# Optimization experiments

Measured on AMD Instinct MI355X. Metric: run time of the kernel, lower is better.

The kernel has to match this reference:

```python
import jax, jax.numpy as jnp
import numpy as np

K = 10          # neighbors, hard-coded in MLP1.forward
NEG_SLOPE = 0.2 # LeakyReLU slope
EPS = 1e-5      # BatchNorm2d default eps


def setup_inputs() -> dict:
    key = jax.random.key(0)
    k1, k2, k3, k4 = jax.random.split(key, 4)
    B, C, N = 8, 6, 4096
    x = jax.random.normal(k1, (B, C, N), dtype=jnp.float32)
    W = jax.random.normal(k2, (64, 6), dtype=jnp.float32) * 0.2      # conv1x1 weight (O, I)
    gamma = jax.random.uniform(k3, (64,), jnp.float32, 0.5, 1.5)     # BN weight
    beta = jax.random.normal(k4, (64,), dtype=jnp.float32) * 0.1     # BN bias
    return {"x": x, "W": W, "gamma": gamma, "beta": beta}


def _knn_idx(x3, k):
    # pairwise_distance[b,i,j] = -||x_i - x_j||^2 (as in the torch knn)
    inner = jnp.einsum('bdn,bdm->bnm', x3, x3)          # x_i . x_j
    xx = jnp.sum(x3 * x3, axis=1)                       # (B, N)
    pd = 2.0 * inner - xx[:, :, None] - xx[:, None, :]  # (B, N, N)
    _, idx = jax.lax.top_k(pd, k)                       # k nearest (incl. self)
    return idx                                          # (B, N, k) int32


def reference(x, W, gamma, beta):
    # x: (B, 6, N)
    idx = _knn_idx(x[:, :3], K)                          # (B, N, k)
    # gather neighbor features: feat[b,c,n,j] = x[b,c,idx[b,n,j]]
    feat = jax.vmap(lambda xb, ib: xb[:, ib])(x, idx)    # (B, 6, N, k)
    # center xyz over the k neighbors and scale by 10
    xyz = feat[:, :3]
    xyz = (xyz - jnp.mean(xyz, axis=-1, keepdims=True)) * 10.0
    feat = jnp.concatenate([xyz, feat[:, 3:]], axis=1)   # (B, 6, N, k)
    # 1x1 conv (6 -> 64), no bias
    y = jnp.einsum('oc,bcnk->bonk', W, feat)             # (B, 64, N, k)
    # BatchNorm2d in train mode: batch stats over (B, N, k), biased variance
    mu = jnp.mean(y, axis=(0, 2, 3), keepdims=True)
    var = jnp.mean((y - mu) ** 2, axis=(0, 2, 3), keepdims=True)
    y = (y - mu) * jax.lax.rsqrt(var + EPS)
    y = y * gamma[None, :, None, None] + beta[None, :, None, None]
    # LeakyReLU(0.2)
    y = jnp.where(y >= 0, y, NEG_SLOPE * y)
    # max over neighbors k
    y = jnp.max(y, axis=-1)                              # (B, 64, N)
    # global max + mean pooling over N, concat along last axis
    x1 = jnp.max(y, axis=-1)                             # (B, 64)
    x2 = jnp.mean(y, axis=-1)                            # (B, 64)
    return jnp.concatenate([x1, x2], axis=-1)            # (B, 128)
```

## Files before the change

kernel.cpp:

```cpp
#include <hip/hip_runtime.h>
#include <float.h>

#define K_NN 10
#define BATCH 8
#define CIN 6
#define NPTS 4096
#define COUT 64
#define NSEG 8
#define SEGLEN (NPTS / NSEG)
#define CHUNK 16
#define NCHUNK (SEGLEN / CHUNK)
#define CAP 32
#define NEG_SLOPE 0.2f
#define BN_EPS 1e-5f

static constexpr size_t OFF_IDX = 0;
static constexpr size_t OFF_PTS = OFF_IDX + (size_t)BATCH * K_NN * NPTS * sizeof(int);
static constexpr size_t OFF_Q   = OFF_PTS + (size_t)BATCH * NPTS * sizeof(float4);
static constexpr size_t SZ_Q    = (size_t)NSEG * BATCH * NPTS * K_NN * sizeof(int);
static constexpr size_t OFF_ST  = OFF_Q + SZ_Q;
static constexpr size_t OFF_SS  = OFF_ST + 32 * sizeof(double);

__device__ __forceinline__ float wave_sum(float v) {
#pragma unroll
    for (int m = 32; m >= 1; m >>= 1) v += __shfl_xor(v, m, 64);
    return v;
}
__device__ __forceinline__ float wave_max(float v) {
#pragma unroll
    for (int m = 32; m >= 1; m >>= 1) v = fmaxf(v, __shfl_xor(v, m, 64));
    return v;
}

__device__ __forceinline__ float distp(float4 qp, float4 c) {
    return fmaf(2.0f, fmaf(qp.z, c.z, fmaf(qp.y, c.y, qp.x * c.x)), -c.w);
}

__global__ __launch_bounds__(256) void prep_pts(const float* __restrict__ x,
                                                float4* __restrict__ pts,
                                                double* __restrict__ stats) {
    if (blockIdx.x == 0 && threadIdx.x < 27) stats[threadIdx.x] = 0.0;
    int t = blockIdx.x * 256 + threadIdx.x;
    int b = t >> 12;
    int n = t & (NPTS - 1);
    const float* xb = x + (size_t)b * CIN * NPTS;
    float x0 = xb[n];
    float x1 = xb[NPTS + n];
    float x2 = xb[2 * NPTS + n];
    pts[t] = make_float4(x0, x1, x2, x0 * x0 + x1 * x1 + x2 * x2);
}

__global__ __launch_bounds__(256) void knn_part(const float4* __restrict__ pts,
                                                int* __restrict__ part) {
    __shared__ unsigned short ssm[CAP * 256];
    int b = blockIdx.y;
    int s = blockIdx.z;
    int n = blockIdx.x * 256 + threadIdx.x;
    const float4* p = pts + (size_t)b * NPTS;
    float4 qp = p[n];

    int m0 = s * SEGLEN;

    float vals[K_NN];
#pragma unroll
    for (int j = 0; j < K_NN; j++) vals[j] = -FLT_MAX;

    for (int ch = 0; ch < NCHUNK; ch++) {
        float cmax = -FLT_MAX;
#pragma unroll
        for (int u = 0; u < CHUNK; u++) {
            float4 c = p[m0 + ch * CHUNK + u];
            cmax = fmaxf(cmax, distp(qp, c));
        }
        float t = cmax;
#pragma unroll
        for (int j = 0; j < K_NN; j++) {
            float hi = fmaxf(vals[j], t);
            t = fminf(vals[j], t);
            vals[j] = hi;
        }
    }
    float thr = vals[K_NN - 1];

    int cnt = 0;
#pragma unroll 8
    for (int mm = 0; mm < SEGLEN; mm++) {
        float4 c = p[m0 + mm];
        float d = distp(qp, c);
        int slot = min(cnt, CAP - 1);
        ssm[slot * 256 + threadIdx.x] = (unsigned short)(m0 + mm);
        cnt += (d >= thr) ? 1 : 0;
    }

    float fv[K_NN];
    int fi[K_NN];
#pragma unroll
    for (int j = 0; j < K_NN; j++) { fv[j] = -FLT_MAX; fi[j] = 0; }

    if (cnt <= CAP) {
        for (int j = 0; j < cnt; j++) {
            int m = ssm[j * 256 + threadIdx.x];
            float4 c = p[m];
            float d = distp(qp, c);
            if (d > fv[K_NN - 1]) {
                fv[K_NN - 1] = d;
                fi[K_NN - 1] = m;
#pragma unroll
                for (int t2 = K_NN - 1; t2 > 0; t2--) {
                    if (fv[t2] > fv[t2 - 1]) {
                        float tv = fv[t2]; fv[t2] = fv[t2 - 1]; fv[t2 - 1] = tv;
                        int ti = fi[t2]; fi[t2] = fi[t2 - 1]; fi[t2 - 1] = ti;
                    }
                }
            }
        }
    } else {
        for (int mm = 0; mm < SEGLEN; mm++) {
            int m = m0 + mm;
            float4 c = p[m];
            float d = distp(qp, c);
            if (d > fv[K_NN - 1]) {
                fv[K_NN - 1] = d;
                fi[K_NN - 1] = m;
#pragma unroll
                for (int t2 = K_NN - 1; t2 > 0; t2--) {
                    if (fv[t2] > fv[t2 - 1]) {
                        float tv = fv[t2]; fv[t2] = fv[t2 - 1]; fv[t2 - 1] = tv;
                        int ti = fi[t2]; fi[t2] = fi[t2 - 1]; fi[t2 - 1] = ti;
                    }
                }
            }
        }
    }

    int* o = part + (((size_t)s * BATCH + b) * K_NN) * NPTS + n;
#pragma unroll
    for (int j = 0; j < K_NN; j++) o[(size_t)j * NPTS] = fi[j];
}

__global__ __launch_bounds__(256) void merge_kernel(const float4* __restrict__ pts,
                                                    const int* __restrict__ part,
                                                    int* __restrict__ idxo) {
    int b = blockIdx.y;
    int n = blockIdx.x * 256 + threadIdx.x;
    const float4* p = pts + (size_t)b * NPTS;
    float4 qp = p[n];

    float vals[K_NN];
    int inds[K_NN];
#pragma unroll
    for (int j = 0; j < K_NN; j++) { vals[j] = -FLT_MAX; inds[j] = 0; }

#pragma unroll
    for (int s = 0; s < NSEG; s++) {
        const int* pp = part + (((size_t)s * BATCH + b) * K_NN) * NPTS + n;
#pragma unroll
        for (int j = 0; j < K_NN; j++) {
            int m = pp[(size_t)j * NPTS];
            float4 c = p[m];
            float d = distp(qp, c);
            if (d > vals[K_NN - 1]) {
                vals[K_NN - 1] = d;
                inds[K_NN - 1] = m;
#pragma unroll
                for (int t = K_NN - 1; t > 0; t--) {
                    if (vals[t] > vals[t - 1]) {
                        float tv = vals[t]; vals[t] = vals[t - 1]; vals[t - 1] = tv;
                        int ti = inds[t]; inds[t] = inds[t - 1]; inds[t - 1] = ti;
                    }
                }
            }
        }
    }

    int* o = idxo + (size_t)b * K_NN * NPTS + n;
#pragma unroll
    for (int j = 0; j < K_NN; j++) o[(size_t)j * NPTS] = inds[j];
}

__global__ __launch_bounds__(256) void feat_kernel(const float4* __restrict__ pts,
                                                   const float* __restrict__ x,
                                                   const float* __restrict__ W,
                                                   const int* __restrict__ idx,
                                                   float* __restrict__ q,
                                                   double* __restrict__ stats) {
    __shared__ float sW[COUT * CIN];
    __shared__ float sred[4][27];
    for (int i = threadIdx.x; i < COUT * CIN; i += 256) sW[i] = W[i];
    __syncthreads();

    int b = blockIdx.y;
    int n = blockIdx.x * 256 + threadIdx.x;
    const float* xb = x + (size_t)b * CIN * NPTS;
    const float4* p = pts + (size_t)b * NPTS;

    int nb[K_NN];
#pragma unroll
    for (int k = 0; k < K_NN; k++) nb[k] = idx[((size_t)b * K_NN + k) * NPTS + n];

    float f[CIN][K_NN];
#pragma unroll
    for (int k = 0; k < K_NN; k++) {
        float4 c = p[nb[k]];
        f[0][k] = c.x; f[1][k] = c.y; f[2][k] = c.z;
    }
#pragma unroll
    for (int c = 3; c < CIN; c++)
#pragma unroll
        for (int k = 0; k < K_NN; k++)
            f[c][k] = xb[c * NPTS + nb[k]];

#pragma unroll
    for (int c = 0; c < 3; c++) {
        float s = 0.f;
#pragma unroll
        for (int k = 0; k < K_NN; k++) s += f[c][k];
        float m = s / 10.0f;
#pragma unroll
        for (int k = 0; k < K_NN; k++) f[c][k] = (f[c][k] - m) * 10.0f;
    }

    float* qb = q + (size_t)b * COUT * NPTS + n;
#pragma unroll
    for (int o = 0; o < COUT; o++) {
        float w0 = sW[o * 6 + 0], w1 = sW[o * 6 + 1], w2 = sW[o * 6 + 2];
        float w3 = sW[o * 6 + 3], w4 = sW[o * 6 + 4], w5 = sW[o * 6 + 5];
        float mx = -FLT_MAX;
#pragma unroll
        for (int k = 0; k < K_NN; k++) {
            float y = w0 * f[0][k] + w1 * f[1][k] + w2 * f[2][k] +
                      w3 * f[3][k] + w4 * f[4][k] + w5 * f[5][k];
            mx = fmaxf(mx, y);
        }
        qb[(size_t)o * NPTS] = mx;
    }

    float s1[CIN];
#pragma unroll
    for (int c = 0; c < CIN; c++) {
        float s = 0.f;
#pragma unroll
        for (int k = 0; k < K_NN; k++) s += f[c][k];
        s1[c] = s;
    }
    float s2[21];
#pragma unroll
    for (int i = 0; i < 21; i++) s2[i] = 0.f;
#pragma unroll
    for (int k = 0; k < K_NN; k++) {
        int pp = 0;
#pragma unroll
        for (int c = 0; c < CIN; c++)
#pragma unroll
            for (int c2 = c; c2 < CIN; c2++) {
                s2[pp] += f[c][k] * f[c2][k];
                pp++;
            }
    }
#pragma unroll
    for (int c = 0; c < CIN; c++) s1[c] = wave_sum(s1[c]);
#pragma unroll
    for (int i = 0; i < 21; i++) s2[i] = wave_sum(s2[i]);

    int wv = threadIdx.x >> 6;
    int ln = threadIdx.x & 63;
    if (ln == 0) {
#pragma unroll
        for (int c = 0; c < CIN; c++) sred[wv][c] = s1[c];
#pragma unroll
        for (int i = 0; i < 21; i++) sred[wv][6 + i] = s2[i];
    }
    __syncthreads();
    if (threadIdx.x < 27) {
        float t = sred[0][threadIdx.x] + sred[1][threadIdx.x] +
                  sred[2][threadIdx.x] + sred[3][threadIdx.x];
        atomicAdd(&stats[threadIdx.x], (double)t);
    }
}

__global__ void stats_kernel(const double* __restrict__ stats,
                             const float* __restrict__ W,
                             const float* __restrict__ gamma,
                             const float* __restrict__ beta,
                             float* __restrict__ ss) {
    int o = threadIdx.x;
    const double minv = 1.0 / (double)((size_t)BATCH * NPTS * K_NN);
    double w[CIN];
#pragma unroll
    for (int c = 0; c < CIN; c++) w[c] = (double)W[o * CIN + c];
    double mu = 0.0;
#pragma unroll
    for (int c = 0; c < CIN; c++) mu += w[c] * stats[c];
    mu *= minv;
    double ey2 = 0.0;
    int p = 6;
#pragma unroll
    for (int c = 0; c < CIN; c++)
#pragma unroll
        for (int c2 = c; c2 < CIN; c2++) {
            double v = w[c] * w[c2] * stats[p];
            ey2 += (c2 == c) ? v : 2.0 * v;
            p++;
        }
    ey2 *= minv;
    double var = ey2 - mu * mu;
    float scale = gamma[o] * rsqrtf((float)var + BN_EPS);
    float shift = beta[o] - (float)mu * scale;
    ss[o] = scale;
    ss[COUT + o] = shift;
}

__global__ __launch_bounds__(256) void reduce_kernel(const float* __restrict__ q,
                                                     const float* __restrict__ ss,
                                                     float* __restrict__ out) {
    int o = blockIdx.x;
    int b = blockIdx.y;
    const float* qp = q + ((size_t)b * COUT + o) * NPTS;
    float scale = ss[o], shift = ss[COUT + o];
    float mx = -FLT_MAX, sm = 0.f;
    for (int i = threadIdx.x; i < NPTS; i += 256) {
        float z = scale * qp[i] + shift;
        z = (z >= 0.f) ? z : NEG_SLOPE * z;
        mx = fmaxf(mx, z);
        sm += z;
    }
    mx = wave_max(mx);
    sm = wave_sum(sm);
    __shared__ float smx[4], ssm2[4];
    int wv = threadIdx.x >> 6;
    int ln = threadIdx.x & 63;
    if (ln == 0) { smx[wv] = mx; ssm2[wv] = sm; }
    __syncthreads();
    if (threadIdx.x == 0) {
        float m = fmaxf(fmaxf(smx[0], smx[1]), fmaxf(smx[2], smx[3]));
        float s = ssm2[0] + ssm2[1] + ssm2[2] + ssm2[3];
        out[b * 2 * COUT + o] = m;
        out[b * 2 * COUT + COUT + o] = s * (1.0f / (float)NPTS);
    }
}

extern "C" void kernel_launch(void* const* d_in, const int* in_sizes, int n_in,
                              void* d_out, int out_size, void* d_ws, size_t ws_size,
                              hipStream_t stream) {
    const float* x     = (const float*)d_in[0];
    const float* W     = (const float*)d_in[1];
    const float* gamma = (const float*)d_in[2];
    const float* beta  = (const float*)d_in[3];
    float* out = (float*)d_out;

    char* ws = (char*)d_ws;
    int*    idx   = (int*)(ws + OFF_IDX);
    float4* pts   = (float4*)(ws + OFF_PTS);
    int*    part  = (int*)(ws + OFF_Q);
    float*  q     = (float*)(ws + OFF_Q);
    double* stats = (double*)(ws + OFF_ST);
    float*  ss    = (float*)(ws + OFF_SS);

    prep_pts<<<BATCH * NPTS / 256, 256, 0, stream>>>(x, pts, stats);
    knn_part<<<dim3(NPTS / 256, BATCH, NSEG), 256, 0, stream>>>(pts, part);
    merge_kernel<<<dim3(NPTS / 256, BATCH), 256, 0, stream>>>(pts, part, idx);
    feat_kernel<<<dim3(NPTS / 256, BATCH), 256, 0, stream>>>(pts, x, W, idx, q, stats);
    stats_kernel<<<1, COUT, 0, stream>>>(stats, W, gamma, beta, ss);
    reduce_kernel<<<dim3(COUT, BATCH), 256, 0, stream>>>(q, ss, out);
}
```

Baseline: 197.5 us.

## Fuse kNN merge into feature kernel with wave-split merging and packed features

```diff
diff --git a/kernel.cpp b/kernel.cpp
--- a/kernel.cpp
+++ b/kernel.cpp
@@ -11,15 +11,16 @@
 #define CHUNK 16
 #define NCHUNK (SEGLEN / CHUNK)
 #define CAP 32
+#define PPB 64
 #define NEG_SLOPE 0.2f
 #define BN_EPS 1e-5f
 
-static constexpr size_t OFF_IDX = 0;
-static constexpr size_t OFF_PTS = OFF_IDX + (size_t)BATCH * K_NN * NPTS * sizeof(int);
-static constexpr size_t OFF_Q   = OFF_PTS + (size_t)BATCH * NPTS * sizeof(float4);
-static constexpr size_t SZ_Q    = (size_t)NSEG * BATCH * NPTS * K_NN * sizeof(int);
-static constexpr size_t OFF_ST  = OFF_Q + SZ_Q;
-static constexpr size_t OFF_SS  = OFF_ST + 32 * sizeof(double);
+static constexpr size_t OFF_PTS2 = 0;
+static constexpr size_t OFF_PTS  = OFF_PTS2 + (size_t)BATCH * NPTS * sizeof(float4);
+static constexpr size_t OFF_Q    = OFF_PTS + (size_t)BATCH * NPTS * sizeof(float4);
+static constexpr size_t SZ_Q     = (size_t)BATCH * NSEG * K_NN * NPTS * sizeof(int);
+static constexpr size_t OFF_ST   = OFF_Q + SZ_Q;
+static constexpr size_t OFF_SS   = OFF_ST + 32 * sizeof(double);
 
 __device__ __forceinline__ float wave_sum(float v) {
 #pragma unroll
@@ -36,8 +37,25 @@
     return fmaf(2.0f, fmaf(qp.z, c.z, fmaf(qp.y, c.y, qp.x * c.x)), -c.w);
 }
 
+__device__ __forceinline__ void lex_insert(float (&vals)[K_NN], int (&inds)[K_NN],
+                                           float d, int m) {
+    if (d > vals[K_NN - 1] || (d == vals[K_NN - 1] && m < inds[K_NN - 1])) {
+        vals[K_NN - 1] = d;
+        inds[K_NN - 1] = m;
+#pragma unroll
+        for (int t = K_NN - 1; t > 0; t--) {
+            if (vals[t] > vals[t - 1] ||
+                (vals[t] == vals[t - 1] && inds[t] < inds[t - 1])) {
+                float tv = vals[t]; vals[t] = vals[t - 1]; vals[t - 1] = tv;
+                int ti = inds[t]; inds[t] = inds[t - 1]; inds[t - 1] = ti;
+            }
+        }
+    }
+}
+
 __global__ __launch_bounds__(256) void prep_pts(const float* __restrict__ x,
                                                 float4* __restrict__ pts,
+                                                float4* __restrict__ pts2,
                                                 double* __restrict__ stats) {
     if (blockIdx.x == 0 && threadIdx.x < 27) stats[threadIdx.x] = 0.0;
     int t = blockIdx.x * 256 + threadIdx.x;
@@ -48,11 +66,12 @@
     float x1 = xb[NPTS + n];
     float x2 = xb[2 * NPTS + n];
     pts[t] = make_float4(x0, x1, x2, x0 * x0 + x1 * x1 + x2 * x2);
+    pts2[t] = make_float4(xb[3 * NPTS + n], xb[4 * NPTS + n], xb[5 * NPTS + n], 0.f);
 }
 
 __global__ __launch_bounds__(256) void knn_part(const float4* __restrict__ pts,
                                                 int* __restrict__ part) {
-    __shared__ unsigned short ssm[CAP * 256];
+    __shared__ unsigned int ssm[CAP * 256];
     int b = blockIdx.y;
     int s = blockIdx.z;
     int n = blockIdx.x * 256 + threadIdx.x;
@@ -88,128 +107,90 @@
         float4 c = p[m0 + mm];
         float d = distp(qp, c);
         int slot = min(cnt, CAP - 1);
-        ssm[slot * 256 + threadIdx.x] = (unsigned short)(m0 + mm);
+        ssm[slot * 256 + threadIdx.x] = (unsigned int)(m0 + mm);
         cnt += (d >= thr) ? 1 : 0;
     }
 
     float fv[K_NN];
     int fi[K_NN];
 #pragma unroll
-    for (int j = 0; j < K_NN; j++) { fv[j] = -FLT_MAX; fi[j] = 0; }
+    for (int j = 0; j < K_NN; j++) { fv[j] = -FLT_MAX; fi[j] = 0x7FFFFFFF; }
 
     if (cnt <= CAP) {
         for (int j = 0; j < cnt; j++) {
-            int m = ssm[j * 256 + threadIdx.x];
+            int m = (int)ssm[j * 256 + threadIdx.x];
             float4 c = p[m];
-            float d = distp(qp, c);
-            if (d > fv[K_NN - 1]) {
-                fv[K_NN - 1] = d;
-                fi[K_NN - 1] = m;
-#pragma unroll
-                for (int t2 = K_NN - 1; t2 > 0; t2--) {
-                    if (fv[t2] > fv[t2 - 1]) {
-                        float tv = fv[t2]; fv[t2] = fv[t2 - 1]; fv[t2 - 1] = tv;
-                        int ti = fi[t2]; fi[t2] = fi[t2 - 1]; fi[t2 - 1] = ti;
-                    }
-                }
-            }
+            lex_insert(fv, fi, distp(qp, c), m);
         }
     } else {
         for (int mm = 0; mm < SEGLEN; mm++) {
             int m = m0 + mm;
             float4 c = p[m];
-            float d = distp(qp, c);
-            if (d > fv[K_NN - 1]) {
-                fv[K_NN - 1] = d;
-                fi[K_NN - 1] = m;
-#pragma unroll
-                for (int t2 = K_NN - 1; t2 > 0; t2--) {
-                    if (fv[t2] > fv[t2 - 1]) {
-                        float tv = fv[t2]; fv[t2] = fv[t2 - 1]; fv[t2 - 1] = tv;
-                        int ti = fi[t2]; fi[t2] = fi[t2 - 1]; fi[t2 - 1] = ti;
-                    }
-                }
-            }
-        }
-    }
-
-    int* o = part + (((size_t)s * BATCH + b) * K_NN) * NPTS + n;
+            lex_insert(fv, fi, distp(qp, c), m);
+        }
+    }
+
+    int* o = part + (((size_t)b * NSEG + s) * K_NN) * NPTS + n;
 #pragma unroll
     for (int j = 0; j < K_NN; j++) o[(size_t)j * NPTS] = fi[j];
 }
 
-__global__ __launch_bounds__(256) void merge_kernel(const float4* __restrict__ pts,
-                                                    const int* __restrict__ part,
-                                                    int* __restrict__ idxo) {
+__global__ __launch_bounds__(256) void merge_feat(const float4* __restrict__ pts,
+                                                  const float4* __restrict__ pts2,
+                                                  const float* __restrict__ W,
+                                                  const int* __restrict__ part,
+                                                  float* __restrict__ q,
+                                                  double* __restrict__ stats) {
+    __shared__ float sW[COUT * CIN];
+    __shared__ float ld[4][K_NN][PPB];
+    __shared__ int   li[4][K_NN][PPB];
+    __shared__ float sred[27];
+    for (int i = threadIdx.x; i < COUT * CIN; i += 256) sW[i] = W[i];
+
     int b = blockIdx.y;
-    int n = blockIdx.x * 256 + threadIdx.x;
+    int pt = threadIdx.x & (PPB - 1);
+    int h = threadIdx.x >> 6;
+    int n = blockIdx.x * PPB + pt;
     const float4* p = pts + (size_t)b * NPTS;
+    const float4* p2 = pts2 + (size_t)b * NPTS;
     float4 qp = p[n];
 
     float vals[K_NN];
     int inds[K_NN];
 #pragma unroll
-    for (int j = 0; j < K_NN; j++) { vals[j] = -FLT_MAX; inds[j] = 0; }
-
-#pragma unroll
-    for (int s = 0; s < NSEG; s++) {
-        const int* pp = part + (((size_t)s * BATCH + b) * K_NN) * NPTS + n;
+    for (int j = 0; j < K_NN; j++) { vals[j] = -FLT_MAX; inds[j] = 0x7FFFFFFF; }
+
+#pragma unroll
+    for (int ss = 0; ss < 2; ss++) {
+        int s = h * 2 + ss;
+        const int* pp = part + (((size_t)b * NSEG + s) * K_NN) * NPTS + n;
 #pragma unroll
         for (int j = 0; j < K_NN; j++) {
             int m = pp[(size_t)j * NPTS];
             float4 c = p[m];
-            float d = distp(qp, c);
-            if (d > vals[K_NN - 1]) {
-                vals[K_NN - 1] = d;
-                inds[K_NN - 1] = m;
-#pragma unroll
-                for (int t = K_NN - 1; t > 0; t--) {
-                    if (vals[t] > vals[t - 1]) {
-                        float tv = vals[t]; vals[t] = vals[t - 1]; vals[t - 1] = tv;
-                        int ti = inds[t]; inds[t] = inds[t - 1]; inds[t - 1] = ti;
-                    }
-                }
-            }
-        }
-    }
-
-    int* o = idxo + (size_t)b * K_NN * NPTS + n;
-#pragma unroll
-    for (int j = 0; j < K_NN; j++) o[(size_t)j * NPTS] = inds[j];
-}
-
-__global__ __launch_bounds__(256) void feat_kernel(const float4* __restrict__ pts,
-                                                   const float* __restrict__ x,
-                                                   const float* __restrict__ W,
-                                                   const int* __restrict__ idx,
-                                                   float* __restrict__ q,
-                                                   double* __restrict__ stats) {
-    __shared__ float sW[COUT * CIN];
-    __shared__ float sred[4][27];
-    for (int i = threadIdx.x; i < COUT * CIN; i += 256) sW[i] = W[i];
+            lex_insert(vals, inds, distp(qp, c), m);
+        }
+    }
+#pragma unroll
+    for (int j = 0; j < K_NN; j++) { ld[h][j][pt] = vals[j]; li[h][j][pt] = inds[j]; }
     __syncthreads();
 
-    int b = blockIdx.y;
-    int n = blockIdx.x * 256 + threadIdx.x;
-    const float* xb = x + (size_t)b * CIN * NPTS;
-    const float4* p = pts + (size_t)b * NPTS;
-
-    int nb[K_NN];
-#pragma unroll
-    for (int k = 0; k < K_NN; k++) nb[k] = idx[((size_t)b * K_NN + k) * NPTS + n];
+#pragma unroll
+    for (int oth = 1; oth < 4; oth++) {
+        int hh = (h + oth) & 3;
+#pragma unroll
+        for (int j = 0; j < K_NN; j++)
+            lex_insert(vals, inds, ld[hh][j][pt], li[hh][j][pt]);
+    }
 
     float f[CIN][K_NN];
 #pragma unroll
     for (int k = 0; k < K_NN; k++) {
-        float4 c = p[nb[k]];
+        float4 c = p[inds[k]];
+        float4 c2 = p2[inds[k]];
         f[0][k] = c.x; f[1][k] = c.y; f[2][k] = c.z;
-    }
-#pragma unroll
-    for (int c = 3; c < CIN; c++)
-#pragma unroll
-        for (int k = 0; k < K_NN; k++)
-            f[c][k] = xb[c * NPTS + nb[k]];
-
+        f[3][k] = c2.x; f[4][k] = c2.y; f[5][k] = c2.z;
+    }
 #pragma unroll
     for (int c = 0; c < 3; c++) {
         float s = 0.f;
@@ -220,9 +201,10 @@
         for (int k = 0; k < K_NN; k++) f[c][k] = (f[c][k] - m) * 10.0f;
     }
 
-    float* qb = q + (size_t)b * COUT * NPTS + n;
-#pragma unroll
-    for (int o = 0; o < COUT; o++) {
+    float* qb = q + (size_t)b * 80 * NPTS + n;
+#pragma unroll
+    for (int oo = 0; oo < 16; oo++) {
+        int o = h * 16 + oo;
         float w0 = sW[o * 6 + 0], w1 = sW[o * 6 + 1], w2 = sW[o * 6 + 2];
         float w3 = sW[o * 6 + 3], w4 = sW[o * 6 + 4], w5 = sW[o * 6 + 5];
         float mx = -FLT_MAX;
@@ -235,46 +217,38 @@
         qb[(size_t)o * NPTS] = mx;
     }
 
-    float s1[CIN];
-#pragma unroll
-    for (int c = 0; c < CIN; c++) {
-        float s = 0.f;
-#pragma unroll
-        for (int k = 0; k < K_NN; k++) s += f[c][k];
-        s1[c] = s;
-    }
-    float s2[21];
-#pragma unroll
-    for (int i = 0; i < 21; i++) s2[i] = 0.f;
-#pragma unroll
-    for (int k = 0; k < K_NN; k++) {
-        int pp = 0;
-#pragma unroll
-        for (int c = 0; c < CIN; c++)
-#pragma unroll
-            for (int c2 = c; c2 < CIN; c2++) {
-                s2[pp] += f[c][k] * f[c2][k];
-                pp++;
-            }
-    }
-#pragma unroll
-    for (int c = 0; c < CIN; c++) s1[c] = wave_sum(s1[c]);
-#pragma unroll
-    for (int i = 0; i < 21; i++) s2[i] = wave_sum(s2[i]);
-
-    int wv = threadIdx.x >> 6;
-    int ln = threadIdx.x & 63;
-    if (ln == 0) {
-#pragma unroll
-        for (int c = 0; c < CIN; c++) sred[wv][c] = s1[c];
-#pragma unroll
-        for (int i = 0; i < 21; i++) sred[wv][6 + i] = s2[i];
-    }
-    __syncthreads();
-    if (threadIdx.x < 27) {
-        float t = sred[0][threadIdx.x] + sred[1][threadIdx.x] +
-                  sred[2][threadIdx.x] + sred[3][threadIdx.x];
-        atomicAdd(&stats[threadIdx.x], (double)t);
+    if (h == 0) {
+        float s1[CIN];
+#pragma unroll
+        for (int c = 0; c < CIN; c++) {
+            float s = 0.f;
+#pragma unroll
+            for (int k = 0; k < K_NN; k++) s += f[c][k];
+            s1[c] = wave_sum(s);
+        }
+        float s2[21];
+#pragma unroll
+        for (int i = 0; i < 21; i++) s2[i] = 0.f;
+#pragma unroll
+        for (int k = 0; k < K_NN; k++) {
+            int pp = 0;
+#pragma unroll
+            for (int c = 0; c < CIN; c++)
+#pragma unroll
+                for (int c2 = c; c2 < CIN; c2++) {
+                    s2[pp] += f[c][k] * f[c2][k];
+                    pp++;
+                }
+        }
+#pragma unroll
+        for (int i = 0; i < 21; i++) s2[i] = wave_sum(s2[i]);
+        if (threadIdx.x == 0) {
+#pragma unroll
+            for (int c = 0; c < CIN; c++) sred[c] = s1[c];
+#pragma unroll
+            for (int i = 0; i < 21; i++) sred[6 + i] = s2[i];
+        }
+        if (threadIdx.x < 27) atomicAdd(&stats[threadIdx.x], (double)sred[threadIdx.x]);
     }
 }
 
@@ -315,7 +289,7 @@
                                                      float* __restrict__ out) {
     int o = blockIdx.x;
     int b = blockIdx.y;
-    const float* qp = q + ((size_t)b * COUT + o) * NPTS;
+    const float* qp = q + ((size_t)b * 80 + o) * NPTS;
     float scale = ss[o], shift = ss[COUT + o];
     float mx = -FLT_MAX, sm = 0.f;
     for (int i = threadIdx.x; i < NPTS; i += 256) {
@@ -349,17 +323,16 @@
     float* out = (float*)d_out;
 
     char* ws = (char*)d_ws;
-    int*    idx   = (int*)(ws + OFF_IDX);
+    float4* pts2  = (float4*)(ws + OFF_PTS2);
     float4* pts   = (float4*)(ws + OFF_PTS);
     int*    part  = (int*)(ws + OFF_Q);
     float*  q     = (float*)(ws + OFF_Q);
     double* stats = (double*)(ws + OFF_ST);
     float*  ss    = (float*)(ws + OFF_SS);
 
-    prep_pts<<<BATCH * NPTS / 256, 256, 0, stream>>>(x, pts, stats);
+    prep_pts<<<BATCH * NPTS / 256, 256, 0, stream>>>(x, pts, pts2, stats);
     knn_part<<<dim3(NPTS / 256, BATCH, NSEG), 256, 0, stream>>>(pts, part);
-    merge_kernel<<<dim3(NPTS / 256, BATCH), 256, 0, stream>>>(pts, part, idx);
-    feat_kernel<<<dim3(NPTS / 256, BATCH), 256, 0, stream>>>(pts, x, W, idx, q, stats);
+    merge_feat<<<dim3(NPTS / PPB, BATCH), 256, 0, stream>>>(pts, pts2, W, part, q, stats);
     stats_kernel<<<1, COUT, 0, stream>>>(stats, W, gamma, beta, ss);
     reduce_kernel<<<dim3(COUT, BATCH), 256, 0, stream>>>(q, ss, out);
 }
```

Result: slower. 210.8 us (+6.7%).
